# Optimization experiments

Hardware: AMD Instinct MI355X
Metric: run time of the kernel (lower is better)

Reference implementation:

```python
import jax, jax.numpy as jnp
import numpy as np

D_MODEL = 1024
D_HIDDEN = 2048
BATCH = 2
SEQ = 4096


def setup_inputs() -> dict:
    key = jax.random.key(0)
    ks = jax.random.split(key, 14)
    d, h = D_MODEL, D_HIDDEN
    s_d = 1.0 / np.sqrt(d)
    s_h = 1.0 / np.sqrt(h)
    x = jax.random.normal(ks[0], (BATCH, SEQ, d), jnp.float32)
    W1 = jax.random.normal(ks[1], (d, d), jnp.float32) * s_d
    W2 = jax.random.normal(ks[2], (d, d), jnp.float32) * s_d
    Wlast = jax.random.normal(ks[3], (d, d), jnp.float32) * s_d
    conv_w = jax.random.normal(ks[4], (d, 1, 3), jnp.float32) * 0.5  # depthwise (O, I/g=1, K)
    conv_b = jnp.zeros((d,), jnp.float32)
    A = jax.random.normal(ks[5], (h,), jnp.float32)
    Wb = jax.random.normal(ks[6], (h, d), jnp.float32) * s_d
    bb = jnp.zeros((h,), jnp.float32)
    Wc = jax.random.normal(ks[7], (d, h), jnp.float32) * s_h
    bc = jnp.zeros((d,), jnp.float32)
    Wd = jax.random.normal(ks[8], (d, d), jnp.float32) * s_d
    bd = jnp.zeros((d,), jnp.float32)
    # small delta so cumsum(delta*A) over SEQ steps stays O(1) (avoids exp overflow)
    Wdelta = jax.random.normal(ks[9], (h, d), jnp.float32) * 0.01
    bdelta = jnp.full((h,), -8.0, jnp.float32)
    return dict(x=x, W1=W1, conv_w=conv_w, conv_b=conv_b, A=A, Wb=Wb, bb=bb,
                Wc=Wc, bc=bc, Wd=Wd, bd=bd, Wdelta=Wdelta, bdelta=bdelta,
                W2=W2, Wlast=Wlast)


def reference(x, W1, conv_w, conv_b, A, Wb, bb, Wc, bc, Wd, bd, Wdelta, bdelta, W2, Wlast):
    # x: [B, L, d]
    x1 = x @ W1.T  # linear1 (no bias)
    # depthwise conv1d, kernel 3, pad 1, groups = d_model
    xc = jax.lax.conv_general_dilated(
        x1.transpose(0, 2, 1), conv_w,
        window_strides=(1,), padding=[(1, 1)],
        feature_group_count=D_MODEL,
        dimension_numbers=('NCH', 'OIH', 'NCH')) + conv_b[None, :, None]
    xa = jax.nn.silu(xc.transpose(0, 2, 1))  # [B, L, d]
    # SSM: delta/A/B discretization + cumprod-cumsum scan along sequence
    delta = jax.nn.softplus(xa @ Wdelta.T + bdelta)  # [B, L, h]
    A_bar = jnp.exp(delta * A)
    B_bar = delta * (xa @ Wb.T + bb)
    A_cum = jnp.cumprod(A_bar, axis=1)
    h_st = jnp.cumsum(B_bar / A_cum, axis=1) * A_cum  # [B, L, h]
    out_ssm = (h_st @ Wc.T + bc) + (xa @ Wd.T + bd)  # [B, L, d]
    # gated residual
    x_res = jax.nn.silu(out_ssm @ W2.T)
    z = out_ssm * x_res
    return out_ssm + z @ Wlast.T
```

## Files before the change

### kernel.cpp

```cpp
#include <hip/hip_runtime.h>
#include <cstdint>
#include <cstddef>

#define DMODEL 1024
#define DH 2048
#define BATCH 2
#define SEQ 4096
#define MROWS (BATCH*SEQ)
#define CHUNK 64
#define NCHUNK (SEQ/CHUNK)

typedef unsigned short u16;
typedef __attribute__((ext_vector_type(8))) short bf16x8;
typedef __attribute__((ext_vector_type(4))) float f32x4;

__device__ __forceinline__ u16 f2bf(float f) {
    union { float f; unsigned u; } v; v.f = f;
    unsigned r = v.u + 0x7FFFu + ((v.u >> 16) & 1u);
    return (u16)(r >> 16);
}
__device__ __forceinline__ float bf2f(u16 h) {
    union { unsigned u; float f; } v; v.u = ((unsigned)h) << 16; return v.f;
}

__device__ __forceinline__ float softplus_fast(float x) {
    if (x < -4.f) return __expf(x);
    return (x > 0.f) ? (x + log1pf(__expf(-x))) : log1pf(__expf(x));
}
__device__ __forceinline__ float silu_fast(float v) {
    return v * __fdividef(1.f, 1.f + __expf(-v));
}

__global__ void cvt_bf16(const float* __restrict__ src, u16* __restrict__ dst, int n4) {
    int i = blockIdx.x * blockDim.x + threadIdx.x;
    if (i >= n4) return;
    const float4 v = reinterpret_cast<const float4*>(src)[i];
    ushort4 o;
    o.x = f2bf(v.x); o.y = f2bf(v.y); o.z = f2bf(v.z); o.w = f2bf(v.w);
    reinterpret_cast<ushort4*>(dst)[i] = o;
}

__device__ __forceinline__ void gload_lds16(const void* g, void* l) {
    __builtin_amdgcn_global_load_lds(
        (const __attribute__((address_space(1))) void*)g,
        (__attribute__((address_space(3))) void*)l,
        16, 0, 0);
}

template<int EP, bool TWOK>
__global__ __launch_bounds__(256, 4) void gemm_bt(
    const u16* __restrict__ A1, const u16* __restrict__ B1, int K1,
    const u16* __restrict__ A2, const u16* __restrict__ B2, int K2,
    float* __restrict__ C, u16* __restrict__ Cb, u16* __restrict__ Cb2,
    const float* __restrict__ bias, const float* __restrict__ bias2,
    const u16* __restrict__ aux,
    int M, int N)
{
    __shared__ __align__(16) char smem[32768];
    u16* As = (u16*)smem;
    u16* Bs = (u16*)(smem + 16384);
    float* ep = (float*)smem;

    const int tid = threadIdx.x;

    const int nwg = gridDim.x * gridDim.y;
    int wg = blockIdx.y * gridDim.x + blockIdx.x;
    wg = (wg & 7) * (nwg >> 3) + (wg >> 3);
    const int stile = wg >> 6;
    const int t64   = wg & 63;
    const int nSn   = gridDim.x >> 3;
    const int sm = (nSn > 0) ? stile / nSn : stile;
    const int sn = (nSn > 0) ? stile - sm * nSn : 0;
    const int m0 = (sm * 8 + (t64 >> 3)) * 128;
    const int n0 = (sn * 8 + (t64 & 7)) * 128;

    const int wave = tid >> 6, lane = tid & 63;
    const int wr = (wave >> 1) * 64;
    const int wc = (wave & 1) * 64;
    const int fr = lane & 15, fq = lane >> 4;

    f32x4 acc[4][4];
    #pragma unroll
    for (int m = 0; m < 4; m++)
        #pragma unroll
        for (int n = 0; n < 4; n++) acc[m][n] = f32x4{0.f, 0.f, 0.f, 0.f};

    const int nt1 = K1 >> 6;
    const int nt  = TWOK ? nt1 + (K2 >> 6) : nt1;

    for (int t = 0; t < nt; ++t) {
        const u16* A = A1; const u16* B = B1; int K = K1; int k0 = t << 6;
        if (TWOK && t >= nt1) { A = A2; B = B2; K = K2; k0 = (t - nt1) << 6; }
        #pragma unroll
        for (int i = 0; i < 4; ++i) {
            const int g = i*256 + tid;
            const int r = g >> 3;
            const int ch = (g & 7) ^ (r & 7);
            gload_lds16(A + (size_t)(m0 + r)*K + (k0 + ch*8), (char*)As + (size_t)g*16);
            gload_lds16(B + (size_t)(n0 + r)*K + (k0 + ch*8), (char*)Bs + (size_t)g*16);
        }
        __syncthreads();

        #pragma unroll
        for (int kk = 0; kk < 2; ++kk) {
            bf16x8 af[4], bfr[4];
            #pragma unroll
            for (int m = 0; m < 4; m++) {
                const int r = wr + m*16 + fr;
                af[m] = *reinterpret_cast<const bf16x8*>(
                    (const char*)As + r*128 + (((kk*4 + fq) ^ (r & 7)) * 16));
            }
            #pragma unroll
            for (int n = 0; n < 4; n++) {
                const int r = wc + n*16 + fr;
                bfr[n] = *reinterpret_cast<const bf16x8*>(
                    (const char*)Bs + r*128 + (((kk*4 + fq) ^ (r & 7)) * 16));
            }
            #pragma unroll
            for (int m = 0; m < 4; m++)
                #pragma unroll
                for (int n = 0; n < 4; n++)
                    acc[m][n] = __builtin_amdgcn_mfma_f32_16x16x32_bf16(af[m], bfr[n], acc[m][n], 0, 0, 0);
        }
        __syncthreads();
    }

    const bool isDelta = (EP == 4) ? (n0 < DH) : false;
    #pragma unroll
    for (int c = 0; c < 4; ++c) {
        if ((wave >> 1) == (c >> 1)) {
            const int mb = (c & 1) * 2;
            #pragma unroll
            for (int mi = 0; mi < 2; mi++) {
                #pragma unroll
                for (int n = 0; n < 4; n++) {
                    const int col = wc + n*16 + fr;
                    #pragma unroll
                    for (int j = 0; j < 4; j++)
                        ep[(mi*16 + fq*4 + j)*132 + col] = acc[mb + mi][n][j];
                }
            }
        }
        __syncthreads();
        #pragma unroll
        for (int p = 0; p < 4; ++p) {
            const int idx = p*256 + tid;
            const int row = idx >> 5, c4 = idx & 31;
            float4 v = *reinterpret_cast<const float4*>(&ep[row*132 + c4*4]);
            const int rg   = m0 + c*32 + row;
            const int colg = n0 + c4*4;
            if constexpr (EP == 4) {
                const int cc = isDelta ? colg : (colg - DH);
                const float4 bv = *reinterpret_cast<const float4*>(
                    (isDelta ? bias : bias2) + cc);
                ushort4 o;
                if (isDelta) {
                    o.x = f2bf(softplus_fast(v.x + bv.x));
                    o.y = f2bf(softplus_fast(v.y + bv.y));
                    o.z = f2bf(softplus_fast(v.z + bv.z));
                    o.w = f2bf(softplus_fast(v.w + bv.w));
                } else {
                    o.x = f2bf(v.x + bv.x); o.y = f2bf(v.y + bv.y);
                    o.z = f2bf(v.z + bv.z); o.w = f2bf(v.w + bv.w);
                }
                *reinterpret_cast<ushort4*>((isDelta ? Cb : Cb2) + (size_t)rg*DH + cc) = o;
            } else {
                if (bias) {
                    const float4 b1 = *reinterpret_cast<const float4*>(bias + colg);
                    v.x += b1.x; v.y += b1.y; v.z += b1.z; v.w += b1.w;
                }
                if (bias2) {
                    const float4 b2 = *reinterpret_cast<const float4*>(bias2 + colg);
                    v.x += b2.x; v.y += b2.y; v.z += b2.z; v.w += b2.w;
                }
                const size_t gidx = (size_t)rg * N + colg;
                if constexpr (EP == 0) {
                    ushort4 o = { f2bf(v.x), f2bf(v.y), f2bf(v.z), f2bf(v.w) };
                    *reinterpret_cast<ushort4*>(Cb + gidx) = o;
                } else if constexpr (EP == 2) {
                    const ushort4 ab = *reinterpret_cast<const ushort4*>(aux + gidx);
                    ushort4 o = { f2bf(bf2f(ab.x) * silu_fast(v.x)),
                                  f2bf(bf2f(ab.y) * silu_fast(v.y)),
                                  f2bf(bf2f(ab.z) * silu_fast(v.z)),
                                  f2bf(bf2f(ab.w) * silu_fast(v.w)) };
                    *reinterpret_cast<ushort4*>(Cb + gidx) = o;
                } else {
                    const ushort4 ab = *reinterpret_cast<const ushort4*>(aux + gidx);
                    float4 o = { bf2f(ab.x) + v.x, bf2f(ab.y) + v.y,
                                 bf2f(ab.z) + v.z, bf2f(ab.w) + v.w };
                    *reinterpret_cast<float4*>(C + gidx) = o;
                }
            }
        }
        __syncthreads();
    }
}

__global__ void conv_silu8(const u16* __restrict__ x1, const float* __restrict__ cw,
                           const float* __restrict__ cb, u16* __restrict__ xab) {
    int t = blockIdx.x * blockDim.x + threadIdx.x;
    int c8  = t & (DMODEL/8 - 1);
    int row = t >> 7;
    int l = row & (SEQ - 1);
    const int c0 = c8 * 8;
    const size_t i0 = (size_t)row * DMODEL + c0;
    bf16x8 v0 = *reinterpret_cast<const bf16x8*>(x1 + i0);
    bf16x8 vm = {}; if (l > 0)       vm = *reinterpret_cast<const bf16x8*>(x1 + i0 - DMODEL);
    bf16x8 vp = {}; if (l < SEQ - 1) vp = *reinterpret_cast<const bf16x8*>(x1 + i0 + DMODEL);
    if (l == 0)       vm = bf16x8{};
    if (l == SEQ - 1) vp = bf16x8{};
    bf16x8 o;
    #pragma unroll
    for (int j = 0; j < 8; ++j) {
        const int c = c0 + j;
        float v = cw[c*3+0]*bf2f((u16)vm[j]) + cw[c*3+1]*bf2f((u16)v0[j])
                + cw[c*3+2]*bf2f((u16)vp[j]) + cb[c];
        o[j] = (short)f2bf(silu_fast(v));
    }
    *reinterpret_cast<bf16x8*>(xab + i0) = o;
}

__global__ void scan_chunks(const u16* __restrict__ delta, const u16* __restrict__ pBv,
                            const float* __restrict__ Avec,
                            float* __restrict__ cA, float* __restrict__ cB) {
    const int c = blockIdx.x * blockDim.x + threadIdx.x;
    const int q = blockIdx.y;
    const int b = blockIdx.z;
    const float Ac = Avec[c];
    float hA = 1.f, hB = 0.f;
    size_t base = ((size_t)b*SEQ + q*CHUNK)*DH + c;
    for (int j = 0; j < CHUNK; ++j) {
        float d = bf2f(delta[base]);
        float Abar = __expf(d * Ac);
        hA *= Abar;
        hB = Abar*hB + d * bf2f(pBv[base]);
        base += DH;
    }
    size_t o = ((size_t)b*NCHUNK + q)*DH + c;
    cA[o] = hA; cB[o] = hB;
}

__global__ void scan_prefix(const float* __restrict__ cA, const float* __restrict__ cB,
                            float* __restrict__ cH) {
    const int t = blockIdx.x * blockDim.x + threadIdx.x;
    const int b = t >> 11;
    const int c = t & (DH - 1);
    float h = 0.f;
    size_t o = ((size_t)b*NCHUNK)*DH + c;
    float a = cA[o], bb = cB[o];
    for (int q = 0; q < NCHUNK; ++q) {
        const size_t on = o + DH;
        float a2 = 0.f, b2 = 0.f;
        if (q + 1 < NCHUNK) { a2 = cA[on]; b2 = cB[on]; }
        cH[o] = h;
        h = a*h + bb;
        a = a2; bb = b2; o = on;
    }
}

__global__ void scan_apply(const u16* __restrict__ delta, const u16* __restrict__ pBv,
                           const float* __restrict__ Avec, const float* __restrict__ cH,
                           u16* __restrict__ hstb) {
    const int c = blockIdx.x * blockDim.x + threadIdx.x;
    const int q = blockIdx.y;
    const int b = blockIdx.z;
    const float Ac = Avec[c];
    float h = cH[((size_t)b*NCHUNK + q)*DH + c];
    size_t base = ((size_t)b*SEQ + q*CHUNK)*DH + c;
    for (int j = 0; j < CHUNK; ++j) {
        float d = bf2f(delta[base]);
        float Abar = __expf(d * Ac);
        h = Abar*h + d * bf2f(pBv[base]);
        hstb[base] = f2bf(h);
        base += DH;
    }
}

extern "C" void kernel_launch(void* const* d_in, const int* in_sizes, int n_in,
                              void* d_out, int out_size, void* d_ws, size_t ws_size,
                              hipStream_t stream) {
    const float* x      = (const float*)d_in[0];
    const float* W1     = (const float*)d_in[1];
    const float* conv_w = (const float*)d_in[2];
    const float* conv_b = (const float*)d_in[3];
    const float* Avec   = (const float*)d_in[4];
    const float* Wb     = (const float*)d_in[5];
    const float* bb     = (const float*)d_in[6];
    const float* Wc     = (const float*)d_in[7];
    const float* bc     = (const float*)d_in[8];
    const float* Wd     = (const float*)d_in[9];
    const float* bd     = (const float*)d_in[10];
    const float* Wdelta = (const float*)d_in[11];
    const float* bdelta = (const float*)d_in[12];
    const float* W2     = (const float*)d_in[13];
    const float* Wlast  = (const float*)d_in[14];
    float* out = (float*)d_out;
    (void)in_sizes; (void)n_in; (void)out_size;

    struct Ptrs {
        u16 *sW;
        float *cA, *cB, *cH;
        u16 *xb, *x1b, *xab, *delta, *pBv, *ossb, *hstb, *zb;
        size_t total;
    };
    auto layout = [&](int passes) -> Ptrs {
        Ptrs P{};
        const size_t Mp = MROWS / passes;
        const int nb = BATCH / passes;
        size_t off = 0;
        auto al = [&](size_t bytes) -> char* {
            char* p = (char*)d_ws + off; off += (bytes + 255) & ~(size_t)255; return p;
        };
        P.sW  = (u16*)al((size_t)2*DH*DMODEL*2);
        P.cA  = (float*)al((size_t)nb*NCHUNK*DH*4);
        P.cB  = (float*)al((size_t)nb*NCHUNK*DH*4);
        P.cH  = (float*)al((size_t)nb*NCHUNK*DH*4);
        char* RA = al(Mp*DMODEL*2);
        char* RB = al(Mp*DMODEL*2);
        char* RC = al(Mp*DMODEL*2);
        char* RD = al(Mp*DH*2);
        char* RE = al(Mp*DH*2);
        char* RF = al(Mp*DH*2);
        P.xb    = (u16*)RA; P.ossb = (u16*)RA;
        P.x1b   = (u16*)RB; P.zb   = (u16*)RB;
        P.xab   = (u16*)RC;
        P.delta = (u16*)RD;
        P.pBv   = (u16*)RE;
        P.hstb  = (u16*)RF;
        P.total = off;
        return P;
    };

    int passes = (ws_size >= layout(1).total) ? 1 : 2;
    Ptrs P = layout(passes);
    if (ws_size < P.total) return;
    const int Mp = MROWS / passes;
    const int nb = BATCH / passes;

    const dim3 blk(256);
    auto cvt = [&](const float* s, u16* d, size_t n) {
        int n4 = (int)(n / 4);
        cvt_bf16<<<dim3((n4 + 255)/256), blk, 0, stream>>>(s, d, n4);
    };
    const dim3 gD (DMODEL/128, Mp/128);
    const dim3 gDB(2*DH/128,   Mp/128);
    u16* sW2 = P.sW + (size_t)DH*DMODEL;

    for (int p = 0; p < passes; ++p) {
        const float* x_p  = x  + (size_t)p*Mp*DMODEL;
        float*      out_p = out + (size_t)p*Mp*DMODEL;

        cvt(x_p, P.xb, (size_t)Mp*DMODEL);
        cvt(W1, P.sW, (size_t)DMODEL*DMODEL);
        gemm_bt<0,false><<<gD, blk, 0, stream>>>(P.xb, P.sW, DMODEL, nullptr, nullptr, 0,
                                                 nullptr, P.x1b, nullptr, nullptr, nullptr, nullptr, Mp, DMODEL);
        conv_silu8<<<dim3(Mp*DMODEL/8/256), blk, 0, stream>>>(P.x1b, conv_w, conv_b, P.xab);
        cvt(Wdelta, P.sW, (size_t)DH*DMODEL);
        cvt(Wb,     sW2,  (size_t)DH*DMODEL);
        gemm_bt<4,false><<<gDB, blk, 0, stream>>>(P.xab, P.sW, DMODEL, nullptr, nullptr, 0,
                                                  nullptr, P.delta, P.pBv, bdelta, bb, nullptr, Mp, 2*DH);
        scan_chunks<<<dim3(DH/256, NCHUNK, nb), blk, 0, stream>>>(P.delta, P.pBv, Avec, P.cA, P.cB);
        scan_prefix<<<dim3(nb*DH/256), blk, 0, stream>>>(P.cA, P.cB, P.cH);
        scan_apply <<<dim3(DH/256, NCHUNK, nb), blk, 0, stream>>>(P.delta, P.pBv, Avec, P.cH, P.hstb);
        cvt(Wd, P.sW, (size_t)DMODEL*DMODEL);
        cvt(Wc, sW2,  (size_t)DMODEL*DH);
        gemm_bt<0,true><<<gD, blk, 0, stream>>>(P.xab, P.sW, DMODEL, P.hstb, sW2, DH,
                                                nullptr, P.ossb, nullptr, bd, bc, nullptr, Mp, DMODEL);
        cvt(W2, P.sW, (size_t)DMODEL*DMODEL);
        gemm_bt<2,false><<<gD, blk, 0, stream>>>(P.ossb, P.sW, DMODEL, nullptr, nullptr, 0,
                                                 nullptr, P.zb, nullptr, nullptr, nullptr, P.ossb, Mp, DMODEL);
        cvt(Wlast, P.sW, (size_t)DMODEL*DMODEL);
        gemm_bt<3,false><<<gD, blk, 0, stream>>>(P.zb, P.sW, DMODEL, nullptr, nullptr, 0,
                                                 out_p, nullptr, nullptr, nullptr, nullptr, P.ossb, Mp, DMODEL);
    }
}
```

Measured before the change: 306.4 us.

## Batch weight conversions, widen GEMM epilogue staging, and vectorize scan kernels

All seven weight casts to bf16 now run in a single multi-tensor kernel into separate buffers, which removes several small launches per pass. The GEMM epilogue stages 64 rows per round in a larger 40KB shared buffer instead of 32, halving the epilogue barrier rounds. The scan kernels each handle two channels per thread with 32-bit loads and stores, halving their thread count and packing the memory accesses. The costs are more workspace, more shared memory per block (which may lower occupancy), and a weight-cast kernel that now runs once per call instead of once per pass.

```diff
diff --git a/kernel.cpp b/kernel.cpp
--- a/kernel.cpp
+++ b/kernel.cpp
@@ -11,6 +11,7 @@
 #define NCHUNK (SEQ/CHUNK)
 
 typedef unsigned short u16;
+typedef unsigned int u32;
 typedef __attribute__((ext_vector_type(8))) short bf16x8;
 typedef __attribute__((ext_vector_type(4))) float f32x4;
 
@@ -38,6 +39,23 @@
     ushort4 o;
     o.x = f2bf(v.x); o.y = f2bf(v.y); o.z = f2bf(v.z); o.w = f2bf(v.w);
     reinterpret_cast<ushort4*>(dst)[i] = o;
+}
+
+struct CvtArgs {
+    const float* src[7];
+    u16* dst[7];
+    unsigned cum[8];
+};
+__global__ void cvt_multi(CvtArgs a) {
+    const unsigned i = blockIdx.x * blockDim.x + threadIdx.x;
+    if (i >= a.cum[7]) return;
+    int s = 0;
+    while (i >= a.cum[s+1]) ++s;
+    const unsigned off = i - a.cum[s];
+    const float4 v = reinterpret_cast<const float4*>(a.src[s])[off];
+    ushort4 o;
+    o.x = f2bf(v.x); o.y = f2bf(v.y); o.z = f2bf(v.z); o.w = f2bf(v.w);
+    reinterpret_cast<ushort4*>(a.dst[s])[off] = o;
 }
 
 __device__ __forceinline__ void gload_lds16(const void* g, void* l) {
@@ -56,7 +74,7 @@
     const u16* __restrict__ aux,
     int M, int N)
 {
-    __shared__ __align__(16) char smem[32768];
+    __shared__ __align__(16) char smem[40960];
     u16* As = (u16*)smem;
     u16* Bs = (u16*)(smem + 16384);
     float* ep = (float*)smem;
@@ -127,27 +145,25 @@
 
     const bool isDelta = (EP == 4) ? (n0 < DH) : false;
     #pragma unroll
-    for (int c = 0; c < 4; ++c) {
-        if ((wave >> 1) == (c >> 1)) {
-            const int mb = (c & 1) * 2;
+    for (int c = 0; c < 2; ++c) {
+        if ((wave >> 1) == c) {
             #pragma unroll
-            for (int mi = 0; mi < 2; mi++) {
+            for (int m = 0; m < 4; m++)
                 #pragma unroll
                 for (int n = 0; n < 4; n++) {
                     const int col = wc + n*16 + fr;
                     #pragma unroll
                     for (int j = 0; j < 4; j++)
-                        ep[(mi*16 + fq*4 + j)*132 + col] = acc[mb + mi][n][j];
+                        ep[(m*16 + fq*4 + j)*132 + col] = acc[m][n][j];
                 }
-            }
         }
         __syncthreads();
         #pragma unroll
-        for (int p = 0; p < 4; ++p) {
+        for (int p = 0; p < 8; ++p) {
             const int idx = p*256 + tid;
             const int row = idx >> 5, c4 = idx & 31;
             float4 v = *reinterpret_cast<const float4*>(&ep[row*132 + c4*4]);
-            const int rg   = m0 + c*32 + row;
+            const int rg   = m0 + c*64 + row;
             const int colg = n0 + c4*4;
             if constexpr (EP == 4) {
                 const int cc = isDelta ? colg : (colg - DH);
@@ -223,21 +239,25 @@
 __global__ void scan_chunks(const u16* __restrict__ delta, const u16* __restrict__ pBv,
                             const float* __restrict__ Avec,
                             float* __restrict__ cA, float* __restrict__ cB) {
-    const int c = blockIdx.x * blockDim.x + threadIdx.x;
+    const int c = (blockIdx.x * blockDim.x + threadIdx.x) * 2;
     const int q = blockIdx.y;
     const int b = blockIdx.z;
-    const float Ac = Avec[c];
-    float hA = 1.f, hB = 0.f;
+    const float A0 = Avec[c], A1 = Avec[c+1];
+    float hA0 = 1.f, hB0 = 0.f, hA1 = 1.f, hB1 = 0.f;
     size_t base = ((size_t)b*SEQ + q*CHUNK)*DH + c;
     for (int j = 0; j < CHUNK; ++j) {
-        float d = bf2f(delta[base]);
-        float Abar = __expf(d * Ac);
-        hA *= Abar;
-        hB = Abar*hB + d * bf2f(pBv[base]);
+        const u32 du = *reinterpret_cast<const u32*>(delta + base);
+        const u32 pu = *reinterpret_cast<const u32*>(pBv + base);
+        const float d0 = bf2f((u16)(du & 0xFFFF)), d1 = bf2f((u16)(du >> 16));
+        const float p0 = bf2f((u16)(pu & 0xFFFF)), p1 = bf2f((u16)(pu >> 16));
+        const float a0 = __expf(d0 * A0), a1 = __expf(d1 * A1);
+        hA0 *= a0; hB0 = a0*hB0 + d0*p0;
+        hA1 *= a1; hB1 = a1*hB1 + d1*p1;
         base += DH;
     }
     size_t o = ((size_t)b*NCHUNK + q)*DH + c;
-    cA[o] = hA; cB[o] = hB;
+    cA[o] = hA0; cA[o+1] = hA1;
+    cB[o] = hB0; cB[o+1] = hB1;
 }
 
 __global__ void scan_prefix(const float* __restrict__ cA, const float* __restrict__ cB,
@@ -261,17 +281,23 @@
 __global__ void scan_apply(const u16* __restrict__ delta, const u16* __restrict__ pBv,
                            const float* __restrict__ Avec, const float* __restrict__ cH,
                            u16* __restrict__ hstb) {
-    const int c = blockIdx.x * blockDim.x + threadIdx.x;
+    const int c = (blockIdx.x * blockDim.x + threadIdx.x) * 2;
     const int q = blockIdx.y;
     const int b = blockIdx.z;
-    const float Ac = Avec[c];
-    float h = cH[((size_t)b*NCHUNK + q)*DH + c];
+    const float A0 = Avec[c], A1 = Avec[c+1];
+    const size_t oh = ((size_t)b*NCHUNK + q)*DH + c;
+    float h0 = cH[oh], h1 = cH[oh+1];
     size_t base = ((size_t)b*SEQ + q*CHUNK)*DH + c;
     for (int j = 0; j < CHUNK; ++j) {
-        float d = bf2f(delta[base]);
-        float Abar = __expf(d * Ac);
-        h = Abar*h + d * bf2f(pBv[base]);
-        hstb[base] = f2bf(h);
+        const u32 du = *reinterpret_cast<const u32*>(delta + base);
+        const u32 pu = *reinterpret_cast<const u32*>(pBv + base);
+        const float d0 = bf2f((u16)(du & 0xFFFF)), d1 = bf2f((u16)(du >> 16));
+        const float p0 = bf2f((u16)(pu & 0xFFFF)), p1 = bf2f((u16)(pu >> 16));
+        const float a0 = __expf(d0 * A0), a1 = __expf(d1 * A1);
+        h0 = a0*h0 + d0*p0;
+        h1 = a1*h1 + d1*p1;
+        const u32 hv = (u32)f2bf(h0) | ((u32)f2bf(h1) << 16);
+        *reinterpret_cast<u32*>(hstb + base) = hv;
         base += DH;
     }
 }
@@ -298,7 +324,7 @@
     (void)in_sizes; (void)n_in; (void)out_size;
 
     struct Ptrs {
-        u16 *sW;
+        u16 *w1, *wdel, *wb, *wd, *wc, *w2, *wl;
         float *cA, *cB, *cH;
         u16 *xb, *x1b, *xab, *delta, *pBv, *ossb, *hstb, *zb;
         size_t total;
@@ -311,7 +337,13 @@
         auto al = [&](size_t bytes) -> char* {
             char* p = (char*)d_ws + off; off += (bytes + 255) & ~(size_t)255; return p;
         };
-        P.sW  = (u16*)al((size_t)2*DH*DMODEL*2);
+        P.w1   = (u16*)al((size_t)DMODEL*DMODEL*2);
+        P.wdel = (u16*)al((size_t)DH*DMODEL*2);
+        P.wb   = (u16*)al((size_t)DH*DMODEL*2);
+        P.wd   = (u16*)al((size_t)DMODEL*DMODEL*2);
+        P.wc   = (u16*)al((size_t)DMODEL*DH*2);
+        P.w2   = (u16*)al((size_t)DMODEL*DMODEL*2);
+        P.wl   = (u16*)al((size_t)DMODEL*DMODEL*2);
         P.cA  = (float*)al((size_t)nb*NCHUNK*DH*4);
         P.cB  = (float*)al((size_t)nb*NCHUNK*DH*4);
         P.cH  = (float*)al((size_t)nb*NCHUNK*DH*4);
@@ -338,39 +370,44 @@
     const int nb = BATCH / passes;
 
     const dim3 blk(256);
-    auto cvt = [&](const float* s, u16* d, size_t n) {
-        int n4 = (int)(n / 4);
-        cvt_bf16<<<dim3((n4 + 255)/256), blk, 0, stream>>>(s, d, n4);
-    };
+
+    {
+        CvtArgs a{};
+        const float* srcs[7] = { W1, Wdelta, Wb, Wd, Wc, W2, Wlast };
+        u16* dsts[7] = { P.w1, P.wdel, P.wb, P.wd, P.wc, P.w2, P.wl };
+        const unsigned n4s[7] = {
+            DMODEL*DMODEL/4, DH*DMODEL/4, DH*DMODEL/4, DMODEL*DMODEL/4,
+            DMODEL*DH/4, DMODEL*DMODEL/4, DMODEL*DMODEL/4 };
+        unsigned cum = 0;
+        for (int s = 0; s < 7; ++s) { a.src[s] = srcs[s]; a.dst[s] = dsts[s]; a.cum[s] = cum; cum += n4s[s]; }
+        a.cum[7] = cum;
+        cvt_multi<<<dim3((cum + 255)/256), blk, 0, stream>>>(a);
+    }
+
     const dim3 gD (DMODEL/128, Mp/128);
     const dim3 gDB(2*DH/128,   Mp/128);
-    u16* sW2 = P.sW + (size_t)DH*DMODEL;
 
     for (int p = 0; p < passes; ++p) {
         const float* x_p  = x  + (size_t)p*Mp*DMODEL;
         float*      out_p = out + (size_t)p*Mp*DMODEL;
 
-        cvt(x_p, P.xb, (size_t)Mp*DMODEL);
-        cvt(W1, P.sW, (size_t)DMODEL*DMODEL);
-        gemm_bt<0,false><<<gD, blk, 0, stream>>>(P.xb, P.sW, DMODEL, nullptr, nullptr, 0,
+        {
+            int n4 = (int)((size_t)Mp*DMODEL / 4);
+            cvt_bf16<<<dim3((n4 + 255)/256), blk, 0, stream>>>(x_p, P.xb, n4);
+        }
+        gemm_bt<0,false><<<gD, blk, 0, stream>>>(P.xb, P.w1, DMODEL, nullptr, nullptr, 0,
                                                  nullptr, P.x1b, nullptr, nullptr, nullptr, nullptr, Mp, DMODEL);
         conv_silu8<<<dim3(Mp*DMODEL/8/256), blk, 0, stream>>>(P.x1b, conv_w, conv_b, P.xab);
-        cvt(Wdelta, P.sW, (size_t)DH*DMODEL);
-        cvt(Wb,     sW2,  (size_t)DH*DMODEL);
-        gemm_bt<4,false><<<gDB, blk, 0, stream>>>(P.xab, P.sW, DMODEL, nullptr, nullptr, 0,
+        gemm_bt<4,false><<<gDB, blk, 0, stream>>>(P.xab, P.wdel, DMODEL, nullptr, nullptr, 0,
                                                   nullptr, P.delta, P.pBv, bdelta, bb, nullptr, Mp, 2*DH);
-        scan_chunks<<<dim3(DH/256, NCHUNK, nb), blk, 0, stream>>>(P.delta, P.pBv, Avec, P.cA, P.cB);
+        scan_chunks<<<dim3(DH/2/256, NCHUNK, nb), blk, 0, stream>>>(P.delta, P.pBv, Avec, P.cA, P.cB);
         scan_prefix<<<dim3(nb*DH/256), blk, 0, stream>>>(P.cA, P.cB, P.cH);
-        scan_apply <<<dim3(DH/256, NCHUNK, nb), blk, 0, stream>>>(P.delta, P.pBv, Avec, P.cH, P.hstb);
-        cvt(Wd, P.sW, (size_t)DMODEL*DMODEL);
-        cvt(Wc, sW2,  (size_t)DMODEL*DH);
-        gemm_bt<0,true><<<gD, blk, 0, stream>>>(P.xab, P.sW, DMODEL, P.hstb, sW2, DH,
+        scan_apply <<<dim3(DH/2/256, NCHUNK, nb), blk, 0, stream>>>(P.delta, P.pBv, Avec, P.cH, P.hstb);
+        gemm_bt<0,true><<<gD, blk, 0, stream>>>(P.xab, P.wd, DMODEL, P.hstb, P.wc, DH,
                                                 nullptr, P.ossb, nullptr, bd, bc, nullptr, Mp, DMODEL);
-        cvt(W2, P.sW, (size_t)DMODEL*DMODEL);
-        gemm_bt<2,false><<<gD, blk, 0, stream>>>(P.ossb, P.sW, DMODEL, nullptr, nullptr, 0,
+        gemm_bt<2,false><<<gD, blk, 0, stream>>>(P.ossb, P.w2, DMODEL, nullptr, nullptr, 0,
                                                  nullptr, P.zb, nullptr, nullptr, nullptr, P.ossb, Mp, DMODEL);
-        cvt(Wlast, P.sW, (size_t)DMODEL*DMODEL);
-        gemm_bt<3,false><<<gD, blk, 0, stream>>>(P.zb, P.sW, DMODEL, nullptr, nullptr, 0,
+        gemm_bt<3,false><<<gD, blk, 0, stream>>>(P.zb, P.wl, DMODEL, nullptr, nullptr, 0,
                                                  out_p, nullptr, nullptr, nullptr, nullptr, P.ossb, Mp, DMODEL);
     }
 }
```

After: 298.7 us. 2.5% less time.
